# Performance work log

Measured on AMD Instinct MI355X. Metric: run time of the kernel, lower is better.

Reference implementation:

```python
import jax, jax.numpy as jnp
import numpy as np

B, N, C = 4, 4096, 128  # batch, tokens (flattened 3D volume), channels
F = 128  # filters


def setup_inputs() -> dict:
    key = jax.random.key(0)
    ks = jax.random.split(key, 7)
    s = 1.0 / np.sqrt(C)
    return {
        "inputs": jax.random.normal(ks[0], (B, N, C), dtype=jnp.float32),
        "Wq": jax.random.normal(ks[1], (C, F), dtype=jnp.float32) * s,
        "bq": jnp.zeros((F,), dtype=jnp.float32),
        "Wk": jax.random.normal(ks[2], (C, F), dtype=jnp.float32) * s,
        "bk": jnp.zeros((F,), dtype=jnp.float32),
        "Wv": jax.random.normal(ks[3], (C, F), dtype=jnp.float32) * s,
        "bv": jnp.zeros((F,), dtype=jnp.float32),
    }


def reference(inputs, Wq, bq, Wk, bk, Wv, bv):
    # Dense projections
    q = inputs @ Wq + bq  # [B, N, F]
    k = inputs @ Wk + bk
    v = inputs @ Wv + bv
    scale = jnp.sqrt(jnp.asarray(F, dtype=q.dtype))
    scores = jnp.einsum("bnf,bmf->bnm", q, k) / scale  # [B, N, N]
    weights = jax.nn.softmax(scores, axis=-1)
    return jnp.einsum("bnm,bmf->bnf", weights, v)
```

## Files before the change

### kernel.cpp

```cpp
#include <hip/hip_runtime.h>

typedef unsigned short u16;
typedef unsigned int u32;
typedef float f32x4 __attribute__((ext_vector_type(4)));
typedef short s16x8 __attribute__((ext_vector_type(8)));
typedef unsigned int u32x2 __attribute__((ext_vector_type(2)));

#define NB 4
#define NT 4096
#define ND 128
#define NQ (NB * NT)

#define QK_SCALE 0.12751879523138906f

using as3_void = __attribute__((address_space(3))) void;
using as1_void = __attribute__((address_space(1))) void;

__device__ __forceinline__ u16 f2bf(float x){
  unsigned u = __float_as_uint(x);
  return (u16)((u + 0x7FFFu + ((u >> 16) & 1u)) >> 16);
}
__device__ __forceinline__ u32 cvtpk(float lo, float hi){
  u32 r; asm("v_cvt_pk_bf16_f32 %0, %1, %2" : "=v"(r) : "v"(lo), "v"(hi)); return r;
}
__device__ __forceinline__ f32x4 mfma16(s16x8 a, s16x8 b, f32x4 c){
  return __builtin_amdgcn_mfma_f32_16x16x32_bf16(a, b, c, 0, 0, 0);
}

__global__ void k_wprep(const float* __restrict__ Wq, const float* __restrict__ Wk,
                        const float* __restrict__ Wv, u16* __restrict__ WT){
  int mat = blockIdx.x >> 7;
  int f   = blockIdx.x & 127;
  const float* W = (mat == 0) ? Wq : (mat == 1) ? Wk : Wv;
  int c = threadIdx.x;
  WT[mat * 16384 + f * 128 + c] = f2bf(W[c * 128 + f]);
}

__global__ __launch_bounds__(256) void k_proj(
    const float* __restrict__ X, const u16* __restrict__ WT,
    const float* __restrict__ bq, const float* __restrict__ bk, const float* __restrict__ bv,
    u16* __restrict__ Qs, u16* __restrict__ Ks, u16* __restrict__ VTs)
{
  const int lane = threadIdx.x & 63;
  const int w    = threadIdx.x >> 6;
  const int lm = lane & 15, lg = lane >> 4;
  const int rowbase = blockIdx.x * 64 + w * 16;

  s16x8 a[4];
  const float* xr = X + (rowbase + lm) * ND;
  #pragma unroll
  for (int kc = 0; kc < 4; ++kc){
    f32x4 x0 = *(const f32x4*)(xr + kc * 32 + lg * 8);
    f32x4 x1 = *(const f32x4*)(xr + kc * 32 + lg * 8 + 4);
    s16x8 t;
    t[0]=(short)f2bf(x0[0]); t[1]=(short)f2bf(x0[1]); t[2]=(short)f2bf(x0[2]); t[3]=(short)f2bf(x0[3]);
    t[4]=(short)f2bf(x1[0]); t[5]=(short)f2bf(x1[1]); t[6]=(short)f2bf(x1[2]); t[7]=(short)f2bf(x1[3]);
    a[kc] = t;
  }

  #pragma unroll
  for (int mat = 0; mat < 3; ++mat){
    const float* bias = (mat==0) ? bq : (mat==1) ? bk : bv;
    float bl[8];
    #pragma unroll
    for (int n = 0; n < 8; ++n) bl[n] = bias[n * 16 + lm];
    f32x4 acc[8];
    #pragma unroll
    for (int n = 0; n < 8; ++n) acc[n] = f32x4{0.f,0.f,0.f,0.f};
    #pragma unroll
    for (int kc = 0; kc < 4; ++kc){
      #pragma unroll
      for (int n = 0; n < 8; ++n){
        s16x8 bf = *(const s16x8*)&WT[mat*16384 + (n*16 + lm)*128 + kc*32 + lg*8];
        acc[n] = mfma16(a[kc], bf, acc[n]);
      }
    }
    #pragma unroll
    for (int n = 0; n < 8; ++n){
      int f = n * 16 + lm;
      #pragma unroll
      for (int i = 0; i < 4; ++i){
        int r = rowbase + lg * 4 + i;
        float val = acc[n][i] + bl[n];
        if (mat == 0){
          Qs[r * ND + f] = f2bf(val * QK_SCALE);
        } else if (mat == 1){
          Ks[r * ND + (f ^ ((r & 7) << 3))] = f2bf(val);
        } else {
          int bb = r >> 12, nt = r & (NT - 1);
          VTs[(bb * ND + f) * NT + (nt ^ ((f & 3) << 3))] = f2bf(val);
        }
      }
    }
  }
}

__global__ __launch_bounds__(512, 2) void k_attn(
    const u16* __restrict__ Qs, const u16* __restrict__ Ks,
    const u16* __restrict__ VTs, float* __restrict__ Out)
{
  __shared__ __align__(16) u16 lds[73728];
  u16* kbuf = lds;
  u16* vbuf = lds + 32768;
  u16* pbuf = lds + 65536;

  const int lin = blockIdx.x;
  const int b   = (lin & 7) >> 1;
  const int qb  = (lin >> 3) + ((lin & 1) << 5);

  const int lane = threadIdx.x & 63;
  const int w  = threadIdx.x >> 6;
  const int g  = w >> 1, qw = w & 1;
  const int lm = lane & 15, lg = lane >> 4;
  const int q0 = b * NT + qb * 64 + qw * 32;

  s16x8 aq[2][4];
  #pragma unroll
  for (int sq = 0; sq < 2; ++sq){
    const u16* qr = Qs + (size_t)(q0 + sq * 16 + lm) * ND;
    #pragma unroll
    for (int kc = 0; kc < 4; ++kc) aq[sq][kc] = *(const s16x8*)(qr + kc * 32 + lg * 8);
  }

  f32x4 o[2][8];
  #pragma unroll
  for (int sq = 0; sq < 2; ++sq)
    #pragma unroll
    for (int n = 0; n < 8; ++n) o[sq][n] = f32x4{0.f,0.f,0.f,0.f};
  float l_[2] = {0.f, 0.f};

  const u16* gk = Ks  + ((size_t)b * NT + g * 1024 + qw * 16 + (lane >> 4)) * ND + (lane & 15) * 8;
  const u16* gv = VTs + ((size_t)b * ND + qw * 64 + (lane >> 2)) * NT + g * 1024 + (lane & 3) * 8;

  auto stage = [&](int par){
    u16* kd = kbuf + par * 16384 + g * 4096 + qw * 2048;
    u16* vd = vbuf + par * 16384 + g * 4096 + qw * 2048;
    #pragma unroll
    for (int j = 0; j < 4; ++j){
      __builtin_amdgcn_global_load_lds((const as1_void*)(gk + (size_t)j * 4 * ND),
                                       (as3_void*)(kd + j * 512), 16, 0, 0);
      __builtin_amdgcn_global_load_lds((const as1_void*)(gv + (size_t)j * 16 * NT),
                                       (as3_void*)(vd + j * 512), 16, 0, 0);
    }
    gk += (size_t)32 * ND;
    gv += 32;
  };

  stage(0);
  __syncthreads();
  int par = 0;

  const int pw = w * 1024;
  const int kswz = (lm & 7) << 3;
  const int vswz = (lm & 3) << 3;
  const int pswz = (lm & 3) << 3;

  for (int t = 0; t < 32; ++t){
    if (t < 31) stage(par ^ 1);
    const u16* kb = kbuf + par * 16384 + g * 4096;
    const u16* vb = vbuf + par * 16384 + g * 4096;

    f32x4 st[2][2];
    #pragma unroll
    for (int sq = 0; sq < 2; ++sq)
      #pragma unroll
      for (int n = 0; n < 2; ++n) st[sq][n] = f32x4{0.f,0.f,0.f,0.f};
    __builtin_amdgcn_s_setprio(1);
    #pragma unroll
    for (int kc = 0; kc < 4; ++kc){
      #pragma unroll
      for (int n = 0; n < 2; ++n){
        s16x8 kf = *(const s16x8*)&kb[(n * 16 + lm) * 128 + ((kc * 32 + lg * 8) ^ kswz)];
        st[0][n] = mfma16(kf, aq[0][kc], st[0][n]);
        st[1][n] = mfma16(kf, aq[1][kc], st[1][n]);
      }
    }
    __builtin_amdgcn_s_setprio(0);

    #pragma unroll
    for (int sq = 0; sq < 2; ++sq){
      #pragma unroll
      for (int n = 0; n < 2; ++n){
        float p0 = __builtin_amdgcn_exp2f(st[sq][n][0]);
        float p1 = __builtin_amdgcn_exp2f(st[sq][n][1]);
        float p2 = __builtin_amdgcn_exp2f(st[sq][n][2]);
        float p3 = __builtin_amdgcn_exp2f(st[sq][n][3]);
        l_[sq] += (p0 + p1) + (p2 + p3);
        *(u32x2*)&pbuf[pw + (sq * 16 + lm) * 32 + ((n * 16 + lg * 4) ^ pswz)] =
            u32x2{cvtpk(p0, p1), cvtpk(p2, p3)};
      }
    }
    asm volatile("s_waitcnt lgkmcnt(0)" ::: "memory");

    s16x8 pa[2];
    #pragma unroll
    for (int sq = 0; sq < 2; ++sq)
      pa[sq] = *(const s16x8*)&pbuf[pw + (sq * 16 + lm) * 32 + ((lg * 8) ^ pswz)];
    __builtin_amdgcn_s_setprio(1);
    #pragma unroll
    for (int nf = 0; nf < 8; ++nf){
      s16x8 vf = *(const s16x8*)&vb[(nf * 16 + lm) * 32 + ((lg * 8) ^ vswz)];
      o[0][nf] = mfma16(pa[0], vf, o[0][nf]);
      o[1][nf] = mfma16(pa[1], vf, o[1][nf]);
    }
    __builtin_amdgcn_s_setprio(0);

    __syncthreads();
    par ^= 1;
  }

  #pragma unroll
  for (int sq = 0; sq < 2; ++sq){
    float v = l_[sq];
    v += __shfl_xor(v, 16);
    v += __shfl_xor(v, 32);
    l_[sq] = v;
  }

  float* mbF = (float*)lds;
  float* lF  = (float*)lds + 24576;
  if (lg == 0){
    lF[g * 64 + qw * 32 + lm]      = l_[0];
    lF[g * 64 + qw * 32 + 16 + lm] = l_[1];
  }
  if (g){
    #pragma unroll
    for (int sq = 0; sq < 2; ++sq){
      #pragma unroll
      for (int i = 0; i < 4; ++i){
        const int row = (g - 1) * 64 + qw * 32 + sq * 16 + lg * 4 + i;
        #pragma unroll
        for (int nf = 0; nf < 8; ++nf)
          mbF[row * 128 + nf * 16 + lm] = o[sq][nf][i];
      }
    }
  }
  __syncthreads();
  if (!g){
    #pragma unroll
    for (int sq = 0; sq < 2; ++sq){
      #pragma unroll
      for (int i = 0; i < 4; ++i){
        const int rloc = qw * 32 + sq * 16 + lg * 4 + i;
        const float inv = 1.f / (lF[rloc] + lF[64 + rloc] + lF[128 + rloc] + lF[192 + rloc]);
        const size_t r = (size_t)(q0 + sq * 16 + lg * 4 + i);
        #pragma unroll
        for (int nf = 0; nf < 8; ++nf){
          const int f = nf * 16 + lm;
          float val = o[sq][nf][i] + mbF[rloc * 128 + f]
                    + mbF[(64 + rloc) * 128 + f] + mbF[(128 + rloc) * 128 + f];
          Out[r * ND + f] = val * inv;
        }
      }
    }
  }
}

extern "C" void kernel_launch(void* const* d_in, const int* in_sizes, int n_in,
                              void* d_out, int out_size, void* d_ws, size_t ws_size,
                              hipStream_t stream) {
  const float* X  = (const float*)d_in[0];
  const float* Wq = (const float*)d_in[1];
  const float* bq = (const float*)d_in[2];
  const float* Wk = (const float*)d_in[3];
  const float* bk = (const float*)d_in[4];
  const float* Wv = (const float*)d_in[5];
  const float* bv = (const float*)d_in[6];
  float* Out = (float*)d_out;

  u16* Qs  = (u16*)d_ws;
  u16* Ks  = Qs  + (size_t)NQ * ND;
  u16* VTs = Ks  + (size_t)NQ * ND;
  u16* WT  = VTs + (size_t)NQ * ND;

  hipLaunchKernelGGL(k_wprep, dim3(3 * 128), dim3(128), 0, stream, Wq, Wk, Wv, WT);
  hipLaunchKernelGGL(k_proj,  dim3(NQ / 64), dim3(256), 0, stream,
                     X, WT, bq, bk, bv, Qs, Ks, VTs);
  hipLaunchKernelGGL(k_attn,  dim3(256), dim3(512), 0, stream, Qs, Ks, VTs, Out);
}
```

Before: 85.85 us.

## Feed softmax probabilities to PV MFMA directly from registers, permuting V layout

Removes the LDS round-trip for the probability tile. Exp outputs are packed straight into the MFMA A-operand, and the V-transpose layout and its LDS read pattern are permuted so the key ordering matches the accumulator layout from the QK MFMA. V is now read as two 8-byte LDS loads per fragment instead of one 16-byte load, and the scratch P buffer is dropped, shrinking LDS. An extra barrier is added before the epilogue reuses LDS.

```diff
diff --git a/kernel.cpp b/kernel.cpp
--- a/kernel.cpp
+++ b/kernel.cpp
@@ -5,6 +5,7 @@
 typedef float f32x4 __attribute__((ext_vector_type(4)));
 typedef short s16x8 __attribute__((ext_vector_type(8)));
 typedef unsigned int u32x2 __attribute__((ext_vector_type(2)));
+typedef unsigned int u32x4 __attribute__((ext_vector_type(4)));
 
 #define NB 4
 #define NT 4096
@@ -88,7 +89,7 @@
           Ks[r * ND + (f ^ ((r & 7) << 3))] = f2bf(val);
         } else {
           int bb = r >> 12, nt = r & (NT - 1);
-          VTs[(bb * ND + f) * NT + (nt ^ ((f & 3) << 3))] = f2bf(val);
+          VTs[(bb * ND + f) * NT + (nt ^ ((f & 3) << 3) ^ (((f >> 2) & 1) << 2))] = f2bf(val);
         }
       }
     }
@@ -99,10 +100,9 @@
     const u16* __restrict__ Qs, const u16* __restrict__ Ks,
     const u16* __restrict__ VTs, float* __restrict__ Out)
 {
-  __shared__ __align__(16) u16 lds[73728];
+  __shared__ __align__(16) u16 lds[65536];
   u16* kbuf = lds;
   u16* vbuf = lds + 32768;
-  u16* pbuf = lds + 65536;
 
   const int lin = blockIdx.x;
   const int b   = (lin & 7) >> 1;
@@ -150,10 +150,10 @@
   __syncthreads();
   int par = 0;
 
-  const int pw = w * 1024;
   const int kswz = (lm & 7) << 3;
-  const int vswz = (lm & 3) << 3;
-  const int pswz = (lm & 3) << 3;
+  const int vswz = ((lm & 3) << 3) ^ (((lm >> 2) & 1) << 2);
+  const int vcol0 = (lg * 4) ^ vswz;
+  const int vcol1 = (16 + lg * 4) ^ vswz;
 
   for (int t = 0; t < 32; ++t){
     if (t < 31) stage(par ^ 1);
@@ -177,29 +177,29 @@
     }
     __builtin_amdgcn_s_setprio(0);
 
+    s16x8 pa[2];
     #pragma unroll
     for (int sq = 0; sq < 2; ++sq){
-      #pragma unroll
-      for (int n = 0; n < 2; ++n){
-        float p0 = __builtin_amdgcn_exp2f(st[sq][n][0]);
-        float p1 = __builtin_amdgcn_exp2f(st[sq][n][1]);
-        float p2 = __builtin_amdgcn_exp2f(st[sq][n][2]);
-        float p3 = __builtin_amdgcn_exp2f(st[sq][n][3]);
-        l_[sq] += (p0 + p1) + (p2 + p3);
-        *(u32x2*)&pbuf[pw + (sq * 16 + lm) * 32 + ((n * 16 + lg * 4) ^ pswz)] =
-            u32x2{cvtpk(p0, p1), cvtpk(p2, p3)};
-      }
-    }
-    asm volatile("s_waitcnt lgkmcnt(0)" ::: "memory");
-
-    s16x8 pa[2];
-    #pragma unroll
-    for (int sq = 0; sq < 2; ++sq)
-      pa[sq] = *(const s16x8*)&pbuf[pw + (sq * 16 + lm) * 32 + ((lg * 8) ^ pswz)];
+      float p[8];
+      #pragma unroll
+      for (int n = 0; n < 2; ++n)
+        #pragma unroll
+        for (int i = 0; i < 4; ++i){
+          p[n * 4 + i] = __builtin_amdgcn_exp2f(st[sq][n][i]);
+          l_[sq] += p[n * 4 + i];
+        }
+      pa[sq] = __builtin_bit_cast(s16x8, u32x4{
+          cvtpk(p[0], p[1]), cvtpk(p[2], p[3]),
+          cvtpk(p[4], p[5]), cvtpk(p[6], p[7])});
+    }
+
     __builtin_amdgcn_s_setprio(1);
     #pragma unroll
     for (int nf = 0; nf < 8; ++nf){
-      s16x8 vf = *(const s16x8*)&vb[(nf * 16 + lm) * 32 + ((lg * 8) ^ vswz)];
+      const int vr = (nf * 16 + lm) * 32;
+      u32x2 v0 = *(const u32x2*)&vb[vr + vcol0];
+      u32x2 v1 = *(const u32x2*)&vb[vr + vcol1];
+      s16x8 vf = __builtin_bit_cast(s16x8, u32x4{v0[0], v0[1], v1[0], v1[1]});
       o[0][nf] = mfma16(pa[0], vf, o[0][nf]);
       o[1][nf] = mfma16(pa[1], vf, o[1][nf]);
     }
@@ -219,6 +219,7 @@
 
   float* mbF = (float*)lds;
   float* lF  = (float*)lds + 24576;
+  __syncthreads();
   if (lg == 0){
     lF[g * 64 + qw * 32 + lm]      = l_[0];
     lF[g * 64 + qw * 32 + 16 + lm] = l_[1];
```

Measured after the change: 79.24 us. 7.7% less time.
